# Kernel optimization log

Hardware: AMD Instinct MI355X
Metric: run time of the kernel (lower is better)

Reference implementation:

```python
import jax, jax.numpy as jnp
import numpy as np

E = 8      # num_expert
D = 1024   # d_model
H = 2048   # expert hidden (htoh4 size)
K = 2      # top_k
N = 2048   # tokens (batch*seq)


def setup_inputs() -> dict:
    key = jax.random.key(0)
    ks = jax.random.split(key, 4)
    sc = lambda k, shape, s: jax.random.normal(k, shape, jnp.float32) * s
    return {
        "inp": jax.random.normal(ks[0], (N, D), jnp.float32),
        "Wg": sc(ks[1], (D, E), D ** -0.5),          # NaiveGate linear
        "bg": jnp.zeros((E,), jnp.float32),
        "W1": sc(ks[2], (E, D, H), D ** -0.5),        # per-expert htoh4
        "b1": jnp.zeros((E, H), jnp.float32),
        "W2": sc(ks[3], (E, H, D), H ** -0.5),        # per-expert h4toh
        "b2": jnp.zeros((E, D), jnp.float32),
    }


def reference(inp, Wg, bg, W1, b1, W2, b2):
    # NaiveGate: linear -> top_k logits -> softmax over the k selected logits
    logits = inp @ Wg + bg                              # [N, E]
    top_val, top_idx = jax.lax.top_k(logits, K)         # [N, K]
    gate_score = jax.nn.softmax(top_val, axis=-1)       # [N, K]

    # Expert grouped compute. Reference computes every expert on every token
    # (exact math, no capacity dropping); combine selects the routed ones.
    h = jax.nn.gelu(jnp.einsum('nd,edh->neh', inp, W1) + b1)   # [N, E, H]
    y = jnp.einsum('neh,ehd->ned', h, W2) + b2                 # [N, E, D]

    # Combine: equivalent to bmm(gate_score[N,1,K], x[N,K,D]) after gather.
    comb = jnp.sum(jax.nn.one_hot(top_idx, E, dtype=inp.dtype)
                   * gate_score[..., None], axis=1)            # [N, E]
    return jnp.einsum('ne,ned->nd', comb, y)                   # [N, D]
```

## Files before the change

kernel.cpp:

```cpp
#include <hip/hip_runtime.h>
#include <math.h>

#define N_TOK 2048
#define DM    1024
#define HD    2048
#define NE    8
#define RMAX  5120
#define TMAX  40
#define KSPL  2

#define GATE_BLKS 512
#define XCVT_BLKS 1024
#define PREP_BLKS (GATE_BLKS + XCVT_BLKS)
#define WCV2_BLKS 512
#define WCV1_BLKS 512

typedef short short8 __attribute__((ext_vector_type(8)));
typedef unsigned short u16x8 __attribute__((ext_vector_type(8)));
typedef float f32x4  __attribute__((ext_vector_type(4)));

__device__ inline unsigned short f2b(float f) {
  unsigned int u = __float_as_uint(f);
  return (unsigned short)((u + 0x7FFFu + ((u >> 16) & 1u)) >> 16);
}
__device__ inline float b2f(unsigned short s) {
  return __uint_as_float(((unsigned int)s) << 16);
}
__device__ inline void gload_lds16(const void* g, void* l) {
  __builtin_amdgcn_global_load_lds(
      (const __attribute__((address_space(1))) unsigned int*)g,
      (__attribute__((address_space(3))) unsigned int*)l, 16, 0, 0);
}

__global__ __launch_bounds__(256) void prep_kernel(
    const float* __restrict__ inp, const float* __restrict__ Wg,
    const float* __restrict__ bg,
    int* __restrict__ top_idx, float* __restrict__ gate_w,
    unsigned short* __restrict__ Xb) {
  int bid = blockIdx.x;
  if (bid < GATE_BLKS) {
    int wave = threadIdx.x >> 6;
    int lane = threadIdx.x & 63;
    int n = bid * 4 + wave;
    float acc[NE];
#pragma unroll
    for (int e = 0; e < NE; ++e) acc[e] = 0.f;
    const float4* wg4 = reinterpret_cast<const float4*>(Wg);
#pragma unroll
    for (int i = 0; i < DM / 64; ++i) {
      int d = i * 64 + lane;
      float x = inp[n * DM + d];
      float4 w0 = wg4[d * 2 + 0];
      float4 w1 = wg4[d * 2 + 1];
      acc[0] += x * w0.x; acc[1] += x * w0.y; acc[2] += x * w0.z; acc[3] += x * w0.w;
      acc[4] += x * w1.x; acc[5] += x * w1.y; acc[6] += x * w1.z; acc[7] += x * w1.w;
    }
#pragma unroll
    for (int off = 32; off > 0; off >>= 1) {
#pragma unroll
      for (int e = 0; e < NE; ++e) acc[e] += __shfl_xor(acc[e], off);
    }
    if (lane == 0) {
      float v0 = -1e30f, v1 = -1e30f; int i0 = -1, i1 = -1;
#pragma unroll
      for (int e = 0; e < NE; ++e) {
        float v = acc[e] + bg[e];
        if (v > v0)      { v1 = v0; i1 = i0; v0 = v; i0 = e; }
        else if (v > v1) { v1 = v;  i1 = e; }
      }
      float e1 = expf(v1 - v0);
      float s  = 1.f + e1;
      top_idx[n * 2]     = i0;
      top_idx[n * 2 + 1] = i1;
      gate_w[n * 2]      = 1.f / s;
      gate_w[n * 2 + 1]  = e1 / s;
    }
  } else {
    int i = ((bid - GATE_BLKS) * 256 + threadIdx.x) * 8;
    float4 a = *(const float4*)(inp + i);
    float4 b = *(const float4*)(inp + i + 4);
    ushort4 pa, pb;
    pa.x = f2b(a.x); pa.y = f2b(a.y); pa.z = f2b(a.z); pa.w = f2b(a.w);
    pb.x = f2b(b.x); pb.y = f2b(b.y); pb.z = f2b(b.z); pb.w = f2b(b.w);
    *(ushort4*)(Xb + i)     = pa;
    *(ushort4*)(Xb + i + 4) = pb;
  }
}

__global__ __launch_bounds__(1024) void wcvt1_kernel(
    const float* __restrict__ W1, unsigned short* __restrict__ W1C) {
  int wb = blockIdx.x;
  int z  = wb >> 6;
  int r  = wb & 63;
  const float* src = W1 + (size_t)z * DM * HD;
  unsigned short* dst = W1C + (size_t)z * DM * HD;
  int n0 = (r & 1) * 1024, k0 = (r >> 1) * 32;
  int t  = threadIdx.x;
  int cg = t & 255, kg = t >> 8;
  const float* s = src + (size_t)(k0 + kg * 8) * HD + n0 + cg * 4;
  float4 v[8];
#pragma unroll
  for (int i = 0; i < 8; ++i) v[i] = *(const float4*)(s + (size_t)i * HD);
#pragma unroll
  for (int c = 0; c < 4; ++c) {
    u16x8 o;
    o[0] = f2b(v[0][c]); o[1] = f2b(v[1][c]); o[2] = f2b(v[2][c]); o[3] = f2b(v[3][c]);
    o[4] = f2b(v[4][c]); o[5] = f2b(v[5][c]); o[6] = f2b(v[6][c]); o[7] = f2b(v[7][c]);
    *(u16x8*)(dst + ((size_t)(k0 / 8 + kg) * HD + n0 + cg * 4 + c) * 8) = o;
  }
}

__global__ __launch_bounds__(1024) void group_kernel(
    const int* __restrict__ top_idx,
    const float* __restrict__ W2,
    int* __restrict__ token_of, int* __restrict__ inv_g,
    int* __restrict__ tile_expert, int* __restrict__ tile_row0,
    int* __restrict__ n_tiles,
    unsigned short* __restrict__ W2C) {
  if (blockIdx.x != 0) {
    int wb = blockIdx.x - 1;
    int z  = wb >> 6;
    int k0 = (wb & 63) * 32;
    const float* src = W2 + (size_t)z * HD * DM;
    unsigned short* dst = W2C + (size_t)z * HD * DM;
    int t  = threadIdx.x;
    int cg = t & 255, kg = t >> 8;
    const float* s = src + (size_t)(k0 + kg * 8) * DM + cg * 4;
    float4 v[8];
#pragma unroll
    for (int i = 0; i < 8; ++i) v[i] = *(const float4*)(s + (size_t)i * DM);
#pragma unroll
    for (int c = 0; c < 4; ++c) {
      u16x8 o;
      o[0] = f2b(v[0][c]); o[1] = f2b(v[1][c]); o[2] = f2b(v[2][c]); o[3] = f2b(v[3][c]);
      o[4] = f2b(v[4][c]); o[5] = f2b(v[5][c]); o[6] = f2b(v[6][c]); o[7] = f2b(v[7][c]);
      *(u16x8*)(dst + ((size_t)(k0 / 8 + kg) * DM + cg * 4 + c) * 8) = o;
    }
    return;
  }
  __shared__ int s_wtot[16];
  int tid = threadIdx.x, lane = tid & 63, wid = tid >> 6;
  int base = 0, tiles = 0;
  for (int e = 0; e < NE; ++e) {
    int cnt = 0;
#pragma unroll
    for (int c0 = 0; c0 < N_TOK; c0 += 1024) {
      int n = c0 + tid;
      int t0 = top_idx[n * 2], t1 = top_idx[n * 2 + 1];
      bool f = (t0 == e) || (t1 == e);
      int k = (t0 == e) ? 0 : 1;
      unsigned long long m = __ballot(f);
      int lp = __popcll(m & ((1ull << lane) - 1ull));
      if (lane == 0) s_wtot[wid] = __popcll(m);
      __syncthreads();
      int wbase = 0, tot = 0;
#pragma unroll
      for (int w = 0; w < 16; ++w) {
        int c = s_wtot[w];
        if (w < wid) wbase += c;
        tot += c;
      }
      if (f) {
        int pos = base + cnt + wbase + lp;
        token_of[pos] = n;
        inv_g[n * 2 + k] = pos;
      }
      cnt += tot;
      __syncthreads();
    }
    int padded = (cnt + 127) & ~127;
    for (int i = cnt + tid; i < padded; i += 1024) token_of[base + i] = -1;
    if (tid == 0) {
      for (int t = 0; t < padded / 128; ++t) {
        tile_expert[tiles + t] = e;
        tile_row0[tiles + t]   = base + t * 128;
      }
    }
    tiles += padded / 128;
    base  += padded;
    __syncthreads();
  }
  if (tid == 0) n_tiles[0] = tiles;
}

__global__ __launch_bounds__(256, 6) void ffn1_mfma(
    const unsigned short* __restrict__ Xb,
    const unsigned short* __restrict__ W1C,
    const float* __restrict__ b1,
    const unsigned short* __restrict__ Xzero,
    const int* __restrict__ token_of, const int* __restrict__ tile_expert,
    const int* __restrict__ tile_row0, const int* __restrict__ n_tiles,
    unsigned short* __restrict__ Hbuf) {
  int lin  = blockIdx.x;
  int xcd  = lin & 7, slot = lin >> 3;
  int unit = xcd * 4 + slot / TMAX;
  int t    = slot % TMAX;
  if (t >= n_tiles[0]) return;
  int e    = tile_expert[t];
  int row0 = tile_row0[t];
  int h0   = unit * 64;
  __shared__ __align__(16) unsigned short Asl[2][128][32];
  __shared__ __align__(16) unsigned short Bsl[2][4][64][8];
  int tid = threadIdx.x, lane = tid & 63;
  int wid = tid >> 6, wr = wid >> 1, wc = wid & 1;
  int l15 = lane & 15, l4 = lane >> 4;
  int sw  = (l15 >> 1) & 3;

  int ar[2], asg[2], tk[2];
#pragma unroll
  for (int q = 0; q < 2; ++q) {
    int idx = tid + q * 256;
    ar[q]  = idx >> 2;
    asg[q] = (idx & 3) ^ ((ar[q] >> 1) & 3);
    tk[q]  = token_of[row0 + ar[q]];
  }
  int bcol = tid & 63, bks = tid >> 6;
  const unsigned short* W1e = W1C + (size_t)e * DM * HD;

  f32x4 acc[4][2] = {};

  auto issueAB = [&](int tt, int buf) {
#pragma unroll
    for (int q = 0; q < 2; ++q) {
      int idx = tid + q * 256;
      const unsigned short* ga = (tk[q] < 0)
          ? Xzero
          : Xb + (size_t)tk[q] * DM + tt * 32 + asg[q] * 8;
      gload_lds16(ga, (char*)&Asl[buf][0][0] + (size_t)idx * 16);
    }
    const unsigned short* gb =
        W1e + ((size_t)(tt * 4 + bks) * HD + h0 + bcol) * 8;
    gload_lds16(gb, (char*)&Bsl[buf][0][0] + (size_t)tid * 16);
  };
  auto compute = [&](int buf) {
    short8 a[4], b[2];
#pragma unroll
    for (int m = 0; m < 4; ++m) {
      int R = wr * 64 + m * 16 + l15;
      a[m] = *(const short8*)((const char*)&Asl[buf][0][0] + R * 64 + ((l4 ^ sw) << 4));
    }
#pragma unroll
    for (int n = 0; n < 2; ++n)
      b[n] = *(const short8*)&Bsl[buf][l4][wc * 32 + n * 16 + l15][0];
#pragma unroll
    for (int m = 0; m < 4; ++m)
#pragma unroll
      for (int n = 0; n < 2; ++n)
        acc[m][n] = __builtin_amdgcn_mfma_f32_16x16x32_bf16(a[m], b[n], acc[m][n], 0, 0, 0);
  };

  issueAB(0, 0);
  for (int kt = 0; kt < 32; kt += 2) {
    __syncthreads();
    if (kt + 1 < 32) issueAB(kt + 1, 1);
    compute(0);
    __syncthreads();
    if (kt + 2 < 32) issueAB(kt + 2, 0);
    compute(1);
  }

  float bias[2];
#pragma unroll
  for (int n = 0; n < 2; ++n) bias[n] = b1[e * HD + h0 + wc * 32 + n * 16 + l15];
#pragma unroll
  for (int m = 0; m < 4; ++m) {
#pragma unroll
    for (int n = 0; n < 2; ++n) {
      int col = h0 + wc * 32 + n * 16 + l15;
#pragma unroll
      for (int j = 0; j < 4; ++j) {
        int row = row0 + wr * 64 + m * 16 + l4 * 4 + j;
        float x = acc[m][n][j] + bias[n];
        float g = 0.5f * x * (1.f + tanhf(0.7978845608f * (x + 0.044715f * x * x * x)));
        Hbuf[(size_t)row * HD + col] = f2b(g);
      }
    }
  }
}

__global__ __launch_bounds__(256, 6) void ffn2_mfma(
    const unsigned short* __restrict__ Hbuf,
    const unsigned short* __restrict__ W2C,
    const float* __restrict__ b2,
    const int* __restrict__ tile_expert, const int* __restrict__ tile_row0,
    const int* __restrict__ n_tiles,
    float* __restrict__ Ypart) {
  int lin  = blockIdx.x;
  int xcd  = lin & 7, slot = lin >> 3;
  int unit = xcd * 4 + slot / TMAX;
  int t    = slot % TMAX;
  if (t >= n_tiles[0]) return;
  int e    = tile_expert[t];
  int row0 = tile_row0[t];
  int d0   = (unit >> 1) * 64;
  int ks   = unit & 1;
  int kbase = ks * (HD / KSPL);
  int kb0   = kbase >> 3;
  __shared__ __align__(16) unsigned short Asl[2][128][32];
  __shared__ __align__(16) unsigned short Bsl[2][4][64][8];
  int tid = threadIdx.x, lane = tid & 63;
  int wid = tid >> 6, wr = wid >> 1, wc = wid & 1;
  int l15 = lane & 15, l4 = lane >> 4;
  int sw  = (l15 >> 1) & 3;

  int ar[2], asg[2];
#pragma unroll
  for (int q = 0; q < 2; ++q) {
    int idx = tid + q * 256;
    ar[q]  = idx >> 2;
    asg[q] = (idx & 3) ^ ((ar[q] >> 1) & 3);
  }
  int bcol = tid & 63, bks = tid >> 6;
  const unsigned short* W2e = W2C + (size_t)e * HD * DM;

  f32x4 acc[4][2] = {};

  auto issueAB = [&](int tt, int buf) {
#pragma unroll
    for (int q = 0; q < 2; ++q) {
      int idx = tid + q * 256;
      const unsigned short* ga =
          Hbuf + (size_t)(row0 + ar[q]) * HD + kbase + tt * 32 + asg[q] * 8;
      gload_lds16(ga, (char*)&Asl[buf][0][0] + (size_t)idx * 16);
    }
    const unsigned short* gb =
        W2e + ((size_t)(kb0 + tt * 4 + bks) * DM + d0 + bcol) * 8;
    gload_lds16(gb, (char*)&Bsl[buf][0][0] + (size_t)tid * 16);
  };
  auto compute = [&](int buf) {
    short8 a[4], b[2];
#pragma unroll
    for (int m = 0; m < 4; ++m) {
      int R = wr * 64 + m * 16 + l15;
      a[m] = *(const short8*)((const char*)&Asl[buf][0][0] + R * 64 + ((l4 ^ sw) << 4));
    }
#pragma unroll
    for (int n = 0; n < 2; ++n)
      b[n] = *(const short8*)&Bsl[buf][l4][wc * 32 + n * 16 + l15][0];
#pragma unroll
    for (int m = 0; m < 4; ++m)
#pragma unroll
      for (int n = 0; n < 2; ++n)
        acc[m][n] = __builtin_amdgcn_mfma_f32_16x16x32_bf16(a[m], b[n], acc[m][n], 0, 0, 0);
  };

  const int NT = HD / KSPL / 32;
  issueAB(0, 0);
  for (int kt = 0; kt < NT; kt += 2) {
    __syncthreads();
    if (kt + 1 < NT) issueAB(kt + 1, 1);
    compute(0);
    __syncthreads();
    if (kt + 2 < NT) issueAB(kt + 2, 0);
    compute(1);
  }

  float bias[2];
#pragma unroll
  for (int n = 0; n < 2; ++n)
    bias[n] = (ks == 0) ? b2[e * DM + d0 + wc * 32 + n * 16 + l15] : 0.f;
  float* Yp = Ypart + (size_t)ks * RMAX * DM;
#pragma unroll
  for (int m = 0; m < 4; ++m) {
#pragma unroll
    for (int n = 0; n < 2; ++n) {
      int col = d0 + wc * 32 + n * 16 + l15;
#pragma unroll
      for (int j = 0; j < 4; ++j) {
        int row = row0 + wr * 64 + m * 16 + l4 * 4 + j;
        Yp[(size_t)row * DM + col] = acc[m][n][j] + bias[n];
      }
    }
  }
}

__global__ void combine_kernel(const float* __restrict__ Ypart,
                               const int* __restrict__ inv_g,
                               const float* __restrict__ gate_w,
                               float* __restrict__ out) {
  int n = blockIdx.x;
  int r0 = inv_g[n * 2], r1 = inv_g[n * 2 + 1];
  float g0 = gate_w[n * 2], g1 = gate_w[n * 2 + 1];
  int i = threadIdx.x;
  const float4* y00 = (const float4*)(Ypart + (size_t)r0 * DM);
  const float4* y01 = (const float4*)(Ypart + (size_t)(RMAX + r0) * DM);
  const float4* y10 = (const float4*)(Ypart + (size_t)r1 * DM);
  const float4* y11 = (const float4*)(Ypart + (size_t)(RMAX + r1) * DM);
  float4 a0 = y00[i], a1 = y01[i], b0 = y10[i], b1 = y11[i];
  float4 rv;
  rv.x = g0 * (a0.x + a1.x) + g1 * (b0.x + b1.x);
  rv.y = g0 * (a0.y + a1.y) + g1 * (b0.y + b1.y);
  rv.z = g0 * (a0.z + a1.z) + g1 * (b0.z + b1.z);
  rv.w = g0 * (a0.w + a1.w) + g1 * (b0.w + b1.w);
  *(float4*)(out + (size_t)n * DM + i * 4) = rv;
}

extern "C" void kernel_launch(void* const* d_in, const int* in_sizes, int n_in,
                              void* d_out, int out_size, void* d_ws, size_t ws_size,
                              hipStream_t stream) {
  const float* inp = (const float*)d_in[0];
  const float* Wg  = (const float*)d_in[1];
  const float* bg  = (const float*)d_in[2];
  const float* W1  = (const float*)d_in[3];
  const float* b1  = (const float*)d_in[4];
  const float* W2  = (const float*)d_in[5];
  const float* b2  = (const float*)d_in[6];
  float* out = (float*)d_out;

  char* ws = (char*)d_ws;
  size_t off = 0;
  auto alloc = [&](size_t bytes) {
    size_t o = off;
    off = (off + bytes + 255) & ~(size_t)255;
    return o;
  };
  int*   top_idx     = (int*)  (ws + alloc(N_TOK * 2 * sizeof(int)));
  float* gate_w      = (float*)(ws + alloc(N_TOK * 2 * sizeof(float)));
  int*   token_of    = (int*)  (ws + alloc(RMAX * sizeof(int)));
  int*   inv_g       = (int*)  (ws + alloc(N_TOK * 2 * sizeof(int)));
  int*   tile_expert = (int*)  (ws + alloc(TMAX * sizeof(int)));
  int*   tile_row0   = (int*)  (ws + alloc(TMAX * sizeof(int)));
  int*   n_tiles     = (int*)  (ws + alloc(sizeof(int)));
  unsigned short* Xzero = (unsigned short*)(ws + alloc(DM * 2));
  unsigned short* Xb    = (unsigned short*)(ws + alloc((size_t)N_TOK * DM * 2));
  unsigned short* W1C   = (unsigned short*)(ws + alloc((size_t)NE * DM * HD * 2));
  unsigned short* W2C   = (unsigned short*)(ws + alloc((size_t)NE * HD * DM * 2));
  unsigned short* Hbuf  = (unsigned short*)(ws + alloc((size_t)RMAX * HD * 2));
  float*          Ypart = (float*)(ws + alloc((size_t)KSPL * RMAX * DM * 4));
  (void)ws_size;

  hipMemsetAsync(Xzero, 0, DM * 2, stream);
  prep_kernel<<<PREP_BLKS, 256, 0, stream>>>(inp, Wg, bg, top_idx, gate_w, Xb);
  wcvt1_kernel<<<WCV1_BLKS, 1024, 0, stream>>>(W1, W1C);
  group_kernel<<<1 + WCV2_BLKS, 1024, 0, stream>>>(
      top_idx, W2, token_of, inv_g, tile_expert, tile_row0, n_tiles, W2C);
  ffn1_mfma<<<8 * 4 * TMAX, 256, 0, stream>>>(
      Xb, W1C, b1, Xzero, token_of, tile_expert, tile_row0, n_tiles, Hbuf);
  ffn2_mfma<<<8 * 4 * TMAX, 256, 0, stream>>>(
      Hbuf, W2C, b2, tile_expert, tile_row0, n_tiles, Ypart);
  combine_kernel<<<N_TOK, 256, 0, stream>>>(Ypart, inv_g, gate_w, out);
}
```

Baseline: 154.6 us.

## Fold W1 conversion into prep kernel and store FFN2 partials in bf16

```diff
diff --git a/kernel.cpp b/kernel.cpp
--- a/kernel.cpp
+++ b/kernel.cpp
@@ -11,9 +11,9 @@
 
 #define GATE_BLKS 512
 #define XCVT_BLKS 1024
-#define PREP_BLKS (GATE_BLKS + XCVT_BLKS)
+#define WCV1_BLKS 2048
+#define PREP_BLKS (GATE_BLKS + XCVT_BLKS + WCV1_BLKS)
 #define WCV2_BLKS 512
-#define WCV1_BLKS 512
 
 typedef short short8 __attribute__((ext_vector_type(8)));
 typedef unsigned short u16x8 __attribute__((ext_vector_type(8)));
@@ -34,9 +34,9 @@
 
 __global__ __launch_bounds__(256) void prep_kernel(
     const float* __restrict__ inp, const float* __restrict__ Wg,
-    const float* __restrict__ bg,
+    const float* __restrict__ bg,  const float* __restrict__ W1,
     int* __restrict__ top_idx, float* __restrict__ gate_w,
-    unsigned short* __restrict__ Xb) {
+    unsigned short* __restrict__ Xb, unsigned short* __restrict__ W1C) {
   int bid = blockIdx.x;
   if (bid < GATE_BLKS) {
     int wave = threadIdx.x >> 6;
@@ -75,7 +75,7 @@
       gate_w[n * 2]      = 1.f / s;
       gate_w[n * 2 + 1]  = e1 / s;
     }
-  } else {
+  } else if (bid < GATE_BLKS + XCVT_BLKS) {
     int i = ((bid - GATE_BLKS) * 256 + threadIdx.x) * 8;
     float4 a = *(const float4*)(inp + i);
     float4 b = *(const float4*)(inp + i + 4);
@@ -84,29 +84,27 @@
     pb.x = f2b(b.x); pb.y = f2b(b.y); pb.z = f2b(b.z); pb.w = f2b(b.w);
     *(ushort4*)(Xb + i)     = pa;
     *(ushort4*)(Xb + i + 4) = pb;
-  }
-}
-
-__global__ __launch_bounds__(1024) void wcvt1_kernel(
-    const float* __restrict__ W1, unsigned short* __restrict__ W1C) {
-  int wb = blockIdx.x;
-  int z  = wb >> 6;
-  int r  = wb & 63;
-  const float* src = W1 + (size_t)z * DM * HD;
-  unsigned short* dst = W1C + (size_t)z * DM * HD;
-  int n0 = (r & 1) * 1024, k0 = (r >> 1) * 32;
-  int t  = threadIdx.x;
-  int cg = t & 255, kg = t >> 8;
-  const float* s = src + (size_t)(k0 + kg * 8) * HD + n0 + cg * 4;
-  float4 v[8];
-#pragma unroll
-  for (int i = 0; i < 8; ++i) v[i] = *(const float4*)(s + (size_t)i * HD);
-#pragma unroll
-  for (int c = 0; c < 4; ++c) {
-    u16x8 o;
-    o[0] = f2b(v[0][c]); o[1] = f2b(v[1][c]); o[2] = f2b(v[2][c]); o[3] = f2b(v[3][c]);
-    o[4] = f2b(v[4][c]); o[5] = f2b(v[5][c]); o[6] = f2b(v[6][c]); o[7] = f2b(v[7][c]);
-    *(u16x8*)(dst + ((size_t)(k0 / 8 + kg) * HD + n0 + cg * 4 + c) * 8) = o;
+  } else {
+    int wb = bid - (GATE_BLKS + XCVT_BLKS);
+    int z  = wb >> 8;
+    int r  = wb & 255;
+    int gx = r & 7, gy = r >> 3;
+    const float* src = W1 + (size_t)z * DM * HD;
+    unsigned short* dst = W1C + (size_t)z * DM * HD;
+    int n0 = gx * 256, k0 = gy * 32;
+    int t  = threadIdx.x;
+    int cg = t & 63, kg = t >> 6;
+    const float* s = src + (size_t)(k0 + kg * 8) * HD + n0 + cg * 4;
+    float4 v[8];
+#pragma unroll
+    for (int i = 0; i < 8; ++i) v[i] = *(const float4*)(s + (size_t)i * HD);
+#pragma unroll
+    for (int c = 0; c < 4; ++c) {
+      u16x8 o;
+      o[0] = f2b(v[0][c]); o[1] = f2b(v[1][c]); o[2] = f2b(v[2][c]); o[3] = f2b(v[3][c]);
+      o[4] = f2b(v[4][c]); o[5] = f2b(v[5][c]); o[6] = f2b(v[6][c]); o[7] = f2b(v[7][c]);
+      *(u16x8*)(dst + ((size_t)(k0 / 8 + kg) * HD + n0 + cg * 4 + c) * 8) = o;
+    }
   }
 }
 
@@ -284,7 +282,7 @@
     const float* __restrict__ b2,
     const int* __restrict__ tile_expert, const int* __restrict__ tile_row0,
     const int* __restrict__ n_tiles,
-    float* __restrict__ Ypart) {
+    unsigned short* __restrict__ Ypart) {
   int lin  = blockIdx.x;
   int xcd  = lin & 7, slot = lin >> 3;
   int unit = xcd * 4 + slot / TMAX;
@@ -359,7 +357,7 @@
 #pragma unroll
   for (int n = 0; n < 2; ++n)
     bias[n] = (ks == 0) ? b2[e * DM + d0 + wc * 32 + n * 16 + l15] : 0.f;
-  float* Yp = Ypart + (size_t)ks * RMAX * DM;
+  unsigned short* Yp = Ypart + (size_t)ks * RMAX * DM;
 #pragma unroll
   for (int m = 0; m < 4; ++m) {
 #pragma unroll
@@ -368,13 +366,13 @@
 #pragma unroll
       for (int j = 0; j < 4; ++j) {
         int row = row0 + wr * 64 + m * 16 + l4 * 4 + j;
-        Yp[(size_t)row * DM + col] = acc[m][n][j] + bias[n];
-      }
-    }
-  }
-}
-
-__global__ void combine_kernel(const float* __restrict__ Ypart,
+        Yp[(size_t)row * DM + col] = f2b(acc[m][n][j] + bias[n]);
+      }
+    }
+  }
+}
+
+__global__ void combine_kernel(const unsigned short* __restrict__ Ypart,
                                const int* __restrict__ inv_g,
                                const float* __restrict__ gate_w,
                                float* __restrict__ out) {
@@ -382,16 +380,21 @@
   int r0 = inv_g[n * 2], r1 = inv_g[n * 2 + 1];
   float g0 = gate_w[n * 2], g1 = gate_w[n * 2 + 1];
   int i = threadIdx.x;
-  const float4* y00 = (const float4*)(Ypart + (size_t)r0 * DM);
-  const float4* y01 = (const float4*)(Ypart + (size_t)(RMAX + r0) * DM);
-  const float4* y10 = (const float4*)(Ypart + (size_t)r1 * DM);
-  const float4* y11 = (const float4*)(Ypart + (size_t)(RMAX + r1) * DM);
-  float4 a0 = y00[i], a1 = y01[i], b0 = y10[i], b1 = y11[i];
+  float s0[4] = {0.f, 0.f, 0.f, 0.f};
+  float s1[4] = {0.f, 0.f, 0.f, 0.f};
+#pragma unroll
+  for (int p = 0; p < KSPL; ++p) {
+    const unsigned short* Yp = Ypart + (size_t)p * RMAX * DM;
+    ushort4 a = *(const ushort4*)(Yp + (size_t)r0 * DM + i * 4);
+    ushort4 b = *(const ushort4*)(Yp + (size_t)r1 * DM + i * 4);
+    s0[0] += b2f(a.x); s0[1] += b2f(a.y); s0[2] += b2f(a.z); s0[3] += b2f(a.w);
+    s1[0] += b2f(b.x); s1[1] += b2f(b.y); s1[2] += b2f(b.z); s1[3] += b2f(b.w);
+  }
   float4 rv;
-  rv.x = g0 * (a0.x + a1.x) + g1 * (b0.x + b1.x);
-  rv.y = g0 * (a0.y + a1.y) + g1 * (b0.y + b1.y);
-  rv.z = g0 * (a0.z + a1.z) + g1 * (b0.z + b1.z);
-  rv.w = g0 * (a0.w + a1.w) + g1 * (b0.w + b1.w);
+  rv.x = g0 * s0[0] + g1 * s1[0];
+  rv.y = g0 * s0[1] + g1 * s1[1];
+  rv.z = g0 * s0[2] + g1 * s1[2];
+  rv.w = g0 * s0[3] + g1 * s1[3];
   *(float4*)(out + (size_t)n * DM + i * 4) = rv;
 }
 
@@ -426,12 +429,12 @@
   unsigned short* W1C   = (unsigned short*)(ws + alloc((size_t)NE * DM * HD * 2));
   unsigned short* W2C   = (unsigned short*)(ws + alloc((size_t)NE * HD * DM * 2));
   unsigned short* Hbuf  = (unsigned short*)(ws + alloc((size_t)RMAX * HD * 2));
-  float*          Ypart = (float*)(ws + alloc((size_t)KSPL * RMAX * DM * 4));
+  unsigned short* Ypart = (unsigned short*)(ws + alloc((size_t)KSPL * RMAX * DM * 2));
   (void)ws_size;
 
   hipMemsetAsync(Xzero, 0, DM * 2, stream);
-  prep_kernel<<<PREP_BLKS, 256, 0, stream>>>(inp, Wg, bg, top_idx, gate_w, Xb);
-  wcvt1_kernel<<<WCV1_BLKS, 1024, 0, stream>>>(W1, W1C);
+  prep_kernel<<<PREP_BLKS, 256, 0, stream>>>(inp, Wg, bg, W1,
+                                             top_idx, gate_w, Xb, W1C);
   group_kernel<<<1 + WCV2_BLKS, 1024, 0, stream>>>(
       top_idx, W2, token_of, inv_g, tile_expert, tile_row0, n_tiles, W2C);
   ffn1_mfma<<<8 * 4 * TMAX, 256, 0, stream>>>(
```

Measured after the change: 142.2 us. 8.0% less time.
